# Kernel tuning notes

Hardware: AMD Instinct MI355X
Metric: run time of the kernel (lower is better)

The kernel has to match this reference:

```python
import jax, jax.numpy as jnp
import numpy as np

N, E = 50000, 800000
DIN, DH, DOUT = 128, 64, 16


def setup_inputs() -> dict:
    key = jax.random.key(0)
    ks = jax.random.split(key, 8)
    s = lambda d: np.float32(1.0 / np.sqrt(d))
    return {
        "x": jax.random.normal(ks[0], (N, DIN), jnp.float32),
        "edge_index": jax.random.randint(ks[1], (2, E), 0, N, dtype=jnp.int32),
        "w0": jax.random.normal(ks[2], (DIN, DH), jnp.float32) * s(DIN),
        "b0": jnp.zeros((DH,), jnp.float32),
        "w1": jax.random.normal(ks[3], (DH, DH), jnp.float32) * s(DH),
        "b1": jnp.zeros((DH,), jnp.float32),
        "w2": jax.random.normal(ks[4], (DH, DH), jnp.float32) * s(DH),
        "b2": jnp.zeros((DH,), jnp.float32),
        "fc_w": jax.random.normal(ks[5], (DH, DOUT), jnp.float32) * s(DH),
        "fc_b": jnp.zeros((DOUT,), jnp.float32),
    }


def reference(x, edge_index, w0, b0, w1, b1, w2, b2, fc_w, fc_b):
    n = x.shape[0]
    loop = jnp.arange(n, dtype=edge_index.dtype)
    # PyG GCNConv default: add self-loops, symmetric normalization
    src = jnp.concatenate([edge_index[0], loop])  # [E+N]
    dst = jnp.concatenate([edge_index[1], loop])
    deg = jax.ops.segment_sum(jnp.ones_like(dst, dtype=x.dtype), dst, num_segments=n)
    dinv = jnp.where(deg > 0, jax.lax.rsqrt(deg), 0.0)
    norm = dinv[src] * dinv[dst]  # [E+N]

    def conv(h, W, b):
        h = h @ W                            # [N, DH]
        msg = h[src] * norm[:, None]         # [E+N, DH] gather + scale
        return jax.ops.segment_sum(msg, dst, num_segments=n) + b

    h = jax.nn.elu(conv(x, w0, b0))
    h = jax.nn.elu(conv(h, w1, b1))
    h = jax.nn.elu(conv(h, w2, b2))
    return jax.nn.softmax(h @ fc_w + fc_b, axis=1)
```

## Files before the change

kernel.cpp:

```cpp
#include <hip/hip_runtime.h>
#include <hip/hip_fp16.h>
#include <math.h>

#define DIN 128
#define DH  64
#define DOUT 16
#define NWIN 8

typedef _Float16 f16x8 __attribute__((ext_vector_type(8)));
typedef float f32x4 __attribute__((ext_vector_type(4)));

__global__ __launch_bounds__(256) void deg_kernel(const int* __restrict__ dst,
                                                  int* __restrict__ counts, int E) {
    int e = blockIdx.x * 256 + threadIdx.x;
    if (e < E) atomicAdd(&counts[dst[e]], 1);
}

__global__ __launch_bounds__(256) void alloc_kernel(const int* __restrict__ counts,
                                                    int* __restrict__ gtotal,
                                                    int* __restrict__ offs,
                                                    int* __restrict__ cursor,
                                                    float* __restrict__ dinv, int n) {
    int i = blockIdx.x * 256 + threadIdx.x;
    if (i >= n) return;
    int c = counts[i];
    int pad = (c + 7) & ~7;
    int o = atomicAdd(gtotal, pad);
    offs[i] = o;
    cursor[i] = o;
    dinv[i] = rsqrtf((float)(c + 1));
}

__global__ __launch_bounds__(256) void fill_kernel(int* __restrict__ a, int v, int cap) {
    int i = blockIdx.x * 256 + threadIdx.x;
    if (i < cap) a[i] = v;
}

__global__ __launch_bounds__(256) void scatter_kernel(const int* __restrict__ src,
                                                      const int* __restrict__ dst,
                                                      int* __restrict__ cursor,
                                                      int* __restrict__ csr_src,
                                                      int E, int winSize) {
    int win = blockIdx.x & (NWIN - 1);
    int group = blockIdx.x >> 3;
    int nGroups = gridDim.x >> 3;
    int lo = win * winSize, hi = lo + winSize;
    int stride = nGroups * 256;
    for (int e = group * 256 + threadIdx.x; e < E; e += stride) {
        int d = dst[e];
        if (d >= lo && d < hi) {
            int j = atomicAdd(&cursor[d], 1);
            csr_src[j] = src[e];
        }
    }
}

__global__ __launch_bounds__(256) void mm128_mfma(const float* __restrict__ H,
                                                  const float* __restrict__ W,
                                                  const float* __restrict__ dinv,
                                                  __half* __restrict__ T, int n, int nTiles) {
    __shared__ _Float16 bhi[4][4][64][8];
    __shared__ _Float16 blo[4][4][64][8];
    int tid = threadIdx.x;
    for (int it = 0; it < 32; ++it) {
        int idx = it * 256 + tid;
        int k = idx >> 6, nn = idx & 63;
        float w = W[idx];
        _Float16 h = (_Float16)w;
        _Float16 l = (_Float16)(w - (float)h);
        int kt = k >> 5, kr = k & 31;
        int g = kr >> 3, j = kr & 7;
        int ct = nn >> 4, c = nn & 15;
        int ln = g * 16 + c;
        bhi[kt][ct][ln][j] = h;
        blo[kt][ct][ln][j] = l;
    }
    if (blockIdx.x == 0 && tid < 64) T[(size_t)n * 64 + tid] = __float2half(0.f);
    __syncthreads();

    int wave = blockIdx.x * 4 + (tid >> 6);
    if (wave >= nTiles) return;
    int lane = tid & 63;
    f16x8 Bh[4][4], Bl[4][4];
    #pragma unroll
    for (int kt = 0; kt < 4; ++kt)
        #pragma unroll
        for (int ct = 0; ct < 4; ++ct) {
            Bh[kt][ct] = *(const f16x8*)&bhi[kt][ct][lane][0];
            Bl[kt][ct] = *(const f16x8*)&blo[kt][ct][lane][0];
        }
    int row0 = wave * 16;
    int arow = row0 + (lane & 15);
    if (arow >= n) arow = n - 1;
    const float* hp = H + (size_t)arow * 128 + ((lane >> 4) << 3);
    f32x4 acc[4];
    #pragma unroll
    for (int ct = 0; ct < 4; ++ct) acc[ct] = (f32x4){0.f, 0.f, 0.f, 0.f};
    #pragma unroll
    for (int kt = 0; kt < 4; ++kt) {
        float4 p0 = *(const float4*)(hp + kt * 32);
        float4 p1 = *(const float4*)(hp + kt * 32 + 4);
        float v[8] = {p0.x, p0.y, p0.z, p0.w, p1.x, p1.y, p1.z, p1.w};
        f16x8 ah, al;
        #pragma unroll
        for (int j = 0; j < 8; ++j) {
            _Float16 h = (_Float16)v[j];
            ah[j] = h;
            al[j] = (_Float16)(v[j] - (float)h);
        }
        #pragma unroll
        for (int ct = 0; ct < 4; ++ct) {
            acc[ct] = __builtin_amdgcn_mfma_f32_16x16x32_f16(ah, Bh[kt][ct], acc[ct], 0, 0, 0);
            acc[ct] = __builtin_amdgcn_mfma_f32_16x16x32_f16(al, Bh[kt][ct], acc[ct], 0, 0, 0);
            acc[ct] = __builtin_amdgcn_mfma_f32_16x16x32_f16(ah, Bl[kt][ct], acc[ct], 0, 0, 0);
        }
    }
    int rbase = row0 + ((lane >> 4) << 2);
    int cbase = lane & 15;
    #pragma unroll
    for (int r = 0; r < 4; ++r) {
        int row = rbase + r;
        if (row < n) {
            float d = dinv[row];
            #pragma unroll
            for (int ct = 0; ct < 4; ++ct)
                T[(size_t)row * 64 + ct * 16 + cbase] = __float2half(acc[ct][r] * d);
        }
    }
}

__global__ __launch_bounds__(256) void aggmm_kernel(const __half* __restrict__ T,
                                                    const int* __restrict__ offs,
                                                    const int* __restrict__ cnt,
                                                    const int* __restrict__ csr_src,
                                                    const float* __restrict__ dinv,
                                                    const float* __restrict__ bias,
                                                    const float* __restrict__ Wn,
                                                    __half* __restrict__ out, int n) {
    __shared__ __align__(16) float wl[64 * 64];
    __shared__ __align__(16) float rowbuf[8][68];
    int tid = threadIdx.x;
    for (int i = tid; i < 64 * 64; i += 256) wl[i] = Wn[i];
    if (blockIdx.x == 0 && tid < 64) out[(size_t)n * 64 + tid] = __float2half(0.f);
    __syncthreads();
    int hw = tid >> 5;
    int f2 = tid & 31;
    int node = blockIdx.x * 8 + hw;
    if (node >= n) return;

    const __half2* T2 = reinterpret_cast<const __half2*>(T);
    float di = dinv[node];
    int e0 = offs[node];
    int e1 = e0 + ((cnt[node] + 7) & ~7);
    float2 sv = __half22float2(T2[(size_t)node * 32 + f2]);
    float ax0 = sv.x, ay0 = sv.y;
    float ax1=0, ay1=0, ax2=0, ay2=0, ax3=0, ay3=0;
    #pragma unroll 1
    for (int e = e0; e < e1; e += 8) {
        int4 sa = *reinterpret_cast<const int4*>(&csr_src[e]);
        int4 sb = *reinterpret_cast<const int4*>(&csr_src[e + 4]);
        float2 v0 = __half22float2(T2[(size_t)sa.x * 32 + f2]);
        float2 v1 = __half22float2(T2[(size_t)sa.y * 32 + f2]);
        float2 v2 = __half22float2(T2[(size_t)sa.z * 32 + f2]);
        float2 v3 = __half22float2(T2[(size_t)sa.w * 32 + f2]);
        float2 v4 = __half22float2(T2[(size_t)sb.x * 32 + f2]);
        float2 v5 = __half22float2(T2[(size_t)sb.y * 32 + f2]);
        float2 v6 = __half22float2(T2[(size_t)sb.z * 32 + f2]);
        float2 v7 = __half22float2(T2[(size_t)sb.w * 32 + f2]);
        ax0 += v0.x + v4.x;  ay0 += v0.y + v4.y;
        ax1 += v1.x + v5.x;  ay1 += v1.y + v5.y;
        ax2 += v2.x + v6.x;  ay2 += v2.y + v6.y;
        ax3 += v3.x + v7.x;  ay3 += v3.y + v7.y;
    }
    float hx = (ax0 + ax1) + (ax2 + ax3);
    float hy = (ay0 + ay1) + (ay2 + ay3);
    float2 bv = *reinterpret_cast<const float2*>(&bias[2 * f2]);
    hx = hx * di + bv.x;
    hy = hy * di + bv.y;
    hx = hx > 0.f ? hx : expm1f(hx);
    hy = hy > 0.f ? hy : expm1f(hy);

    *reinterpret_cast<float2*>(&rowbuf[hw][2 * f2]) = make_float2(hx, hy);
    float ox = 0.f, oy = 0.f;
    #pragma unroll
    for (int k0 = 0; k0 < 64; k0 += 4) {
        float4 r4 = *reinterpret_cast<const float4*>(&rowbuf[hw][k0]);
        float2 w0 = *reinterpret_cast<const float2*>(&wl[(k0 + 0) * 64 + 2 * f2]);
        float2 w1 = *reinterpret_cast<const float2*>(&wl[(k0 + 1) * 64 + 2 * f2]);
        float2 w2 = *reinterpret_cast<const float2*>(&wl[(k0 + 2) * 64 + 2 * f2]);
        float2 w3 = *reinterpret_cast<const float2*>(&wl[(k0 + 3) * 64 + 2 * f2]);
        ox = fmaf(r4.x, w0.x, ox); oy = fmaf(r4.x, w0.y, oy);
        ox = fmaf(r4.y, w1.x, ox); oy = fmaf(r4.y, w1.y, oy);
        ox = fmaf(r4.z, w2.x, ox); oy = fmaf(r4.z, w2.y, oy);
        ox = fmaf(r4.w, w3.x, ox); oy = fmaf(r4.w, w3.y, oy);
    }
    __half2* out2 = reinterpret_cast<__half2*>(out);
    out2[(size_t)node * 32 + f2] = __float22half2_rn(make_float2(ox * di, oy * di));
}

__global__ __launch_bounds__(256) void aggfc_kernel(const __half* __restrict__ T,
                                                    const int* __restrict__ offs,
                                                    const int* __restrict__ cnt,
                                                    const int* __restrict__ csr_src,
                                                    const float* __restrict__ dinv,
                                                    const float* __restrict__ bias,
                                                    const float* __restrict__ fcw,
                                                    const float* __restrict__ fcb,
                                                    float* __restrict__ out, int n) {
    __shared__ __align__(16) float wl[64 * 17];
    __shared__ __align__(16) float rowbuf[8][68];
    int tid = threadIdx.x;
    for (int i = tid; i < 64 * 16; i += 256) {
        int k = i >> 4, j = i & 15;
        wl[k * 17 + j] = fcw[i];
    }
    __syncthreads();
    int hw = tid >> 5, f2 = tid & 31;
    int node = blockIdx.x * 8 + hw;
    if (node >= n) return;

    const __half2* T2 = reinterpret_cast<const __half2*>(T);
    float di = dinv[node];
    int e0 = offs[node];
    int e1 = e0 + ((cnt[node] + 7) & ~7);
    float2 sv = __half22float2(T2[(size_t)node * 32 + f2]);
    float ax0 = sv.x, ay0 = sv.y;
    float ax1=0, ay1=0, ax2=0, ay2=0, ax3=0, ay3=0;
    #pragma unroll 1
    for (int e = e0; e < e1; e += 8) {
        int4 sa = *reinterpret_cast<const int4*>(&csr_src[e]);
        int4 sb = *reinterpret_cast<const int4*>(&csr_src[e + 4]);
        float2 v0 = __half22float2(T2[(size_t)sa.x * 32 + f2]);
        float2 v1 = __half22float2(T2[(size_t)sa.y * 32 + f2]);
        float2 v2 = __half22float2(T2[(size_t)sa.z * 32 + f2]);
        float2 v3 = __half22float2(T2[(size_t)sa.w * 32 + f2]);
        float2 v4 = __half22float2(T2[(size_t)sb.x * 32 + f2]);
        float2 v5 = __half22float2(T2[(size_t)sb.y * 32 + f2]);
        float2 v6 = __half22float2(T2[(size_t)sb.z * 32 + f2]);
        float2 v7 = __half22float2(T2[(size_t)sb.w * 32 + f2]);
        ax0 += v0.x + v4.x;  ay0 += v0.y + v4.y;
        ax1 += v1.x + v5.x;  ay1 += v1.y + v5.y;
        ax2 += v2.x + v6.x;  ay2 += v2.y + v6.y;
        ax3 += v3.x + v7.x;  ay3 += v3.y + v7.y;
    }
    float hx = (ax0 + ax1) + (ax2 + ax3);
    float hy = (ay0 + ay1) + (ay2 + ay3);
    float2 bv = *reinterpret_cast<const float2*>(&bias[2 * f2]);
    hx = hx * di + bv.x;
    hy = hy * di + bv.y;
    hx = hx > 0.f ? hx : expm1f(hx);
    hy = hy > 0.f ? hy : expm1f(hy);
    *reinterpret_cast<float2*>(&rowbuf[hw][2 * f2]) = make_float2(hx, hy);

    int g = f2 >> 4;
    int j = f2 & 15;
    float o = 0.f;
    #pragma unroll
    for (int kk = 0; kk < 32; ++kk) {
        int k = g * 32 + kk;
        o += rowbuf[hw][k] * wl[k * 17 + j];
    }
    o += __shfl_xor(o, 16, 64);
    o += fcb[j];
    float m = o;
    #pragma unroll
    for (int d = 8; d; d >>= 1) m = fmaxf(m, __shfl_xor(m, d, 64));
    float ex = expf(o - m);
    float s = ex;
    #pragma unroll
    for (int d = 8; d; d >>= 1) s += __shfl_xor(s, d, 64);
    if ((f2 & 16) == 0) out[(size_t)node * 16 + j] = ex / s;
}

extern "C" void kernel_launch(void* const* d_in, const int* in_sizes, int n_in,
                              void* d_out, int out_size, void* d_ws, size_t ws_size,
                              hipStream_t stream) {
    const float* x   = (const float*)d_in[0];
    const int*   ei  = (const int*)d_in[1];
    const float* w0  = (const float*)d_in[2];
    const float* b0  = (const float*)d_in[3];
    const float* w1  = (const float*)d_in[4];
    const float* b1  = (const float*)d_in[5];
    const float* w2  = (const float*)d_in[6];
    const float* b2  = (const float*)d_in[7];
    const float* fcw = (const float*)d_in[8];
    const float* fcb = (const float*)d_in[9];
    float* out = (float*)d_out;

    const int N = in_sizes[0] / DIN;
    const int E = in_sizes[1] / 2;
    const int* src = ei;
    const int* dst = ei + E;
    const int csr_cap = E + 8 * N + 8;

    char* p = (char*)d_ws;
    auto take = [&](size_t bytes) {
        char* q = p;
        p += (bytes + 255) & ~(size_t)255;
        return q;
    };
    int*    counts  = (int*)take((size_t)(N + 1) * 4);
    int*    gtotal  = counts + N;
    int*    offs    = (int*)take((size_t)N * 4);
    int*    cursor  = (int*)take((size_t)N * 4);
    float*  dinv    = (float*)take((size_t)N * 4);
    int*    csr_src = (int*)take((size_t)csr_cap * 4);
    __half* tbufA   = (__half*)take((size_t)(N + 1) * DH * 2);
    __half* tbufB   = (__half*)take((size_t)(N + 1) * DH * 2);

    hipMemsetAsync(counts, 0, (size_t)(N + 1) * 4, stream);

    deg_kernel<<<(E + 255) / 256, 256, 0, stream>>>(dst, counts, E);
    alloc_kernel<<<(N + 255) / 256, 256, 0, stream>>>(counts, gtotal, offs, cursor, dinv, N);
    fill_kernel<<<(csr_cap + 255) / 256, 256, 0, stream>>>(csr_src, N, csr_cap);
    int winSize = (N + NWIN - 1) / NWIN;
    scatter_kernel<<<1024, 256, 0, stream>>>(src, dst, cursor, csr_src, E, winSize);

    int node_grid = (N + 7) / 8;
    int nTiles = (N + 15) / 16;

    mm128_mfma<<<(nTiles + 3) / 4, 256, 0, stream>>>(x, w0, dinv, tbufA, N, nTiles);
    aggmm_kernel<<<node_grid, 256, 0, stream>>>(tbufA, offs, counts, csr_src,
                                                dinv, b0, w1, tbufB, N);
    aggmm_kernel<<<node_grid, 256, 0, stream>>>(tbufB, offs, counts, csr_src,
                                                dinv, b1, w2, tbufA, N);
    aggfc_kernel<<<node_grid, 256, 0, stream>>>(tbufA, offs, counts, csr_src,
                                                dinv, b2, fcw, fcb, out, N);
}
```

Before: 278.2 us.

## Split feature tables into column halves and gather each half separately

Splits each transformed feature table into two 32-column fp16 halves stored in separate buffers, so every gather pass touches a 3.2 MB table that can stay resident in cache instead of a 6.4 MB one. Aggregation is split in two: one kernel gathers the first half into an fp32 scratch buffer, and a second kernel gathers the other half, combines both, applies ELU and runs the next layer's matmul on MFMA (split fp16 hi/lo) over 64-node tiles. The final layer's FC and softmax also move to MFMA. This doubles the passes over the CSR index array, adds extra kernel launches and an fp32 scratch round-trip, and uses nontemporal hints on the index loads.

```diff
diff --git a/kernel.cpp b/kernel.cpp
--- a/kernel.cpp
+++ b/kernel.cpp
@@ -2,13 +2,12 @@
 #include <hip/hip_fp16.h>
 #include <math.h>
 
-#define DIN 128
-#define DH  64
-#define DOUT 16
 #define NWIN 8
 
 typedef _Float16 f16x8 __attribute__((ext_vector_type(8)));
 typedef float f32x4 __attribute__((ext_vector_type(4)));
+
+__device__ __forceinline__ float eluf(float v) { return v > 0.f ? v : expm1f(v); }
 
 __global__ __launch_bounds__(256) void deg_kernel(const int* __restrict__ dst,
                                                   int* __restrict__ counts, int E) {
@@ -58,7 +57,9 @@
 __global__ __launch_bounds__(256) void mm128_mfma(const float* __restrict__ H,
                                                   const float* __restrict__ W,
                                                   const float* __restrict__ dinv,
-                                                  __half* __restrict__ T, int n, int nTiles) {
+                                                  __half* __restrict__ TA,
+                                                  __half* __restrict__ TB,
+                                                  int n, int nTiles) {
     __shared__ _Float16 bhi[4][4][64][8];
     __shared__ _Float16 blo[4][4][64][8];
     int tid = threadIdx.x;
@@ -71,11 +72,13 @@
         int kt = k >> 5, kr = k & 31;
         int g = kr >> 3, j = kr & 7;
         int ct = nn >> 4, c = nn & 15;
-        int ln = g * 16 + c;
-        bhi[kt][ct][ln][j] = h;
-        blo[kt][ct][ln][j] = l;
-    }
-    if (blockIdx.x == 0 && tid < 64) T[(size_t)n * 64 + tid] = __float2half(0.f);
+        bhi[kt][ct][g * 16 + c][j] = h;
+        blo[kt][ct][g * 16 + c][j] = l;
+    }
+    if (blockIdx.x == 0 && tid < 32) {
+        TA[n * 32 + tid] = __float2half(0.f);
+        TB[n * 32 + tid] = __float2half(0.f);
+    }
     __syncthreads();
 
     int wave = blockIdx.x * 4 + (tid >> 6);
@@ -123,153 +126,311 @@
         if (row < n) {
             float d = dinv[row];
             #pragma unroll
-            for (int ct = 0; ct < 4; ++ct)
-                T[(size_t)row * 64 + ct * 16 + cbase] = __float2half(acc[ct][r] * d);
-        }
-    }
-}
-
-__global__ __launch_bounds__(256) void aggmm_kernel(const __half* __restrict__ T,
-                                                    const int* __restrict__ offs,
-                                                    const int* __restrict__ cnt,
-                                                    const int* __restrict__ csr_src,
-                                                    const float* __restrict__ dinv,
-                                                    const float* __restrict__ bias,
-                                                    const float* __restrict__ Wn,
-                                                    __half* __restrict__ out, int n) {
-    __shared__ __align__(16) float wl[64 * 64];
-    __shared__ __align__(16) float rowbuf[8][68];
-    int tid = threadIdx.x;
-    for (int i = tid; i < 64 * 64; i += 256) wl[i] = Wn[i];
-    if (blockIdx.x == 0 && tid < 64) out[(size_t)n * 64 + tid] = __float2half(0.f);
-    __syncthreads();
-    int hw = tid >> 5;
-    int f2 = tid & 31;
-    int node = blockIdx.x * 8 + hw;
+            for (int ct = 0; ct < 4; ++ct) {
+                int col = ct * 16 + cbase;
+                __half* P = (col < 32) ? TA : TB;
+                P[row * 32 + (col & 31)] = __float2half(acc[ct][r] * d);
+            }
+        }
+    }
+}
+
+__global__ __launch_bounds__(256) void gatherA_kernel(const __half* __restrict__ P,
+                                                      const int* __restrict__ offs,
+                                                      const int* __restrict__ cnt,
+                                                      const int* __restrict__ csr_src,
+                                                      float* __restrict__ agg, int n) {
+    int t = blockIdx.x * 256 + threadIdx.x;
+    int node = t >> 4, l = t & 15;
     if (node >= n) return;
-
-    const __half2* T2 = reinterpret_cast<const __half2*>(T);
-    float di = dinv[node];
+    const __half2* P2 = (const __half2*)P;
+    float2 sv = __half22float2(P2[node * 16 + l]);
+    float ax0 = sv.x, ay0 = sv.y;
+    float ax1 = 0, ay1 = 0, ax2 = 0, ay2 = 0, ax3 = 0, ay3 = 0;
     int e0 = offs[node];
     int e1 = e0 + ((cnt[node] + 7) & ~7);
-    float2 sv = __half22float2(T2[(size_t)node * 32 + f2]);
-    float ax0 = sv.x, ay0 = sv.y;
-    float ax1=0, ay1=0, ax2=0, ay2=0, ax3=0, ay3=0;
     #pragma unroll 1
     for (int e = e0; e < e1; e += 8) {
-        int4 sa = *reinterpret_cast<const int4*>(&csr_src[e]);
-        int4 sb = *reinterpret_cast<const int4*>(&csr_src[e + 4]);
-        float2 v0 = __half22float2(T2[(size_t)sa.x * 32 + f2]);
-        float2 v1 = __half22float2(T2[(size_t)sa.y * 32 + f2]);
-        float2 v2 = __half22float2(T2[(size_t)sa.z * 32 + f2]);
-        float2 v3 = __half22float2(T2[(size_t)sa.w * 32 + f2]);
-        float2 v4 = __half22float2(T2[(size_t)sb.x * 32 + f2]);
-        float2 v5 = __half22float2(T2[(size_t)sb.y * 32 + f2]);
-        float2 v6 = __half22float2(T2[(size_t)sb.z * 32 + f2]);
-        float2 v7 = __half22float2(T2[(size_t)sb.w * 32 + f2]);
+        int s0 = __builtin_nontemporal_load(csr_src + e);
+        int s1 = __builtin_nontemporal_load(csr_src + e + 1);
+        int s2 = __builtin_nontemporal_load(csr_src + e + 2);
+        int s3 = __builtin_nontemporal_load(csr_src + e + 3);
+        int s4 = __builtin_nontemporal_load(csr_src + e + 4);
+        int s5 = __builtin_nontemporal_load(csr_src + e + 5);
+        int s6 = __builtin_nontemporal_load(csr_src + e + 6);
+        int s7 = __builtin_nontemporal_load(csr_src + e + 7);
+        float2 v0 = __half22float2(P2[s0 * 16 + l]);
+        float2 v1 = __half22float2(P2[s1 * 16 + l]);
+        float2 v2 = __half22float2(P2[s2 * 16 + l]);
+        float2 v3 = __half22float2(P2[s3 * 16 + l]);
+        float2 v4 = __half22float2(P2[s4 * 16 + l]);
+        float2 v5 = __half22float2(P2[s5 * 16 + l]);
+        float2 v6 = __half22float2(P2[s6 * 16 + l]);
+        float2 v7 = __half22float2(P2[s7 * 16 + l]);
         ax0 += v0.x + v4.x;  ay0 += v0.y + v4.y;
         ax1 += v1.x + v5.x;  ay1 += v1.y + v5.y;
         ax2 += v2.x + v6.x;  ay2 += v2.y + v6.y;
         ax3 += v3.x + v7.x;  ay3 += v3.y + v7.y;
     }
-    float hx = (ax0 + ax1) + (ax2 + ax3);
-    float hy = (ay0 + ay1) + (ay2 + ay3);
-    float2 bv = *reinterpret_cast<const float2*>(&bias[2 * f2]);
-    hx = hx * di + bv.x;
-    hy = hy * di + bv.y;
-    hx = hx > 0.f ? hx : expm1f(hx);
-    hy = hy > 0.f ? hy : expm1f(hy);
-
-    *reinterpret_cast<float2*>(&rowbuf[hw][2 * f2]) = make_float2(hx, hy);
-    float ox = 0.f, oy = 0.f;
-    #pragma unroll
-    for (int k0 = 0; k0 < 64; k0 += 4) {
-        float4 r4 = *reinterpret_cast<const float4*>(&rowbuf[hw][k0]);
-        float2 w0 = *reinterpret_cast<const float2*>(&wl[(k0 + 0) * 64 + 2 * f2]);
-        float2 w1 = *reinterpret_cast<const float2*>(&wl[(k0 + 1) * 64 + 2 * f2]);
-        float2 w2 = *reinterpret_cast<const float2*>(&wl[(k0 + 2) * 64 + 2 * f2]);
-        float2 w3 = *reinterpret_cast<const float2*>(&wl[(k0 + 3) * 64 + 2 * f2]);
-        ox = fmaf(r4.x, w0.x, ox); oy = fmaf(r4.x, w0.y, oy);
-        ox = fmaf(r4.y, w1.x, ox); oy = fmaf(r4.y, w1.y, oy);
-        ox = fmaf(r4.z, w2.x, ox); oy = fmaf(r4.z, w2.y, oy);
-        ox = fmaf(r4.w, w3.x, ox); oy = fmaf(r4.w, w3.y, oy);
-    }
-    __half2* out2 = reinterpret_cast<__half2*>(out);
-    out2[(size_t)node * 32 + f2] = __float22half2_rn(make_float2(ox * di, oy * di));
-}
-
-__global__ __launch_bounds__(256) void aggfc_kernel(const __half* __restrict__ T,
-                                                    const int* __restrict__ offs,
-                                                    const int* __restrict__ cnt,
-                                                    const int* __restrict__ csr_src,
-                                                    const float* __restrict__ dinv,
-                                                    const float* __restrict__ bias,
-                                                    const float* __restrict__ fcw,
-                                                    const float* __restrict__ fcb,
-                                                    float* __restrict__ out, int n) {
-    __shared__ __align__(16) float wl[64 * 17];
-    __shared__ __align__(16) float rowbuf[8][68];
+    float rx = (ax0 + ax1) + (ax2 + ax3);
+    float ry = (ay0 + ay1) + (ay2 + ay3);
+    __builtin_nontemporal_store(rx, agg + node * 32 + 2 * l);
+    __builtin_nontemporal_store(ry, agg + node * 32 + 2 * l + 1);
+}
+
+__global__ __launch_bounds__(256, 4) void gatherB_mm(const __half* __restrict__ PB,
+                                                     const float* __restrict__ agg,
+                                                     const int* __restrict__ offs,
+                                                     const int* __restrict__ cnt,
+                                                     const int* __restrict__ csr_src,
+                                                     const float* __restrict__ dinv,
+                                                     const float* __restrict__ bias,
+                                                     const float* __restrict__ Wn,
+                                                     __half* __restrict__ outA,
+                                                     __half* __restrict__ outB, int n) {
+    __shared__ _Float16 bhi[2][4][64][8];
+    __shared__ _Float16 blo[2][4][64][8];
+    __shared__ float rowbuf[64][68];
     int tid = threadIdx.x;
-    for (int i = tid; i < 64 * 16; i += 256) {
-        int k = i >> 4, j = i & 15;
-        wl[k * 17 + j] = fcw[i];
+    for (int it = 0; it < 16; ++it) {
+        int idx = it * 256 + tid;
+        int k = idx >> 6, nn = idx & 63;
+        float w = Wn[idx];
+        _Float16 h = (_Float16)w;
+        _Float16 lo = (_Float16)(w - (float)h);
+        int kt = k >> 5, kr = k & 31;
+        int g = kr >> 3, j = kr & 7;
+        int ct = nn >> 4, c = nn & 15;
+        bhi[kt][ct][g * 16 + c][j] = h;
+        blo[kt][ct][g * 16 + c][j] = lo;
+    }
+    if (blockIdx.x == 0 && tid < 32) {
+        outA[n * 32 + tid] = __float2half(0.f);
+        outB[n * 32 + tid] = __float2half(0.f);
+    }
+    int g16 = tid >> 4, l = tid & 15;
+    int nodebase = blockIdx.x * 64;
+    const __half2* P2 = (const __half2*)PB;
+    #pragma unroll 1
+    for (int q = 0; q < 4; ++q) {
+        int ln = 4 * g16 + q;
+        int node = nodebase + ln;
+        float h0 = 0.f, h1 = 0.f, h2 = 0.f, h3 = 0.f;
+        if (node < n) {
+            float2 sv = __half22float2(P2[node * 16 + l]);
+            float ax0 = sv.x, ay0 = sv.y;
+            float ax1 = 0, ay1 = 0, ax2 = 0, ay2 = 0, ax3 = 0, ay3 = 0;
+            int e0 = offs[node];
+            int e1 = e0 + ((cnt[node] + 7) & ~7);
+            #pragma unroll 1
+            for (int e = e0; e < e1; e += 8) {
+                int s0 = __builtin_nontemporal_load(csr_src + e);
+                int s1 = __builtin_nontemporal_load(csr_src + e + 1);
+                int s2 = __builtin_nontemporal_load(csr_src + e + 2);
+                int s3 = __builtin_nontemporal_load(csr_src + e + 3);
+                int s4 = __builtin_nontemporal_load(csr_src + e + 4);
+                int s5 = __builtin_nontemporal_load(csr_src + e + 5);
+                int s6 = __builtin_nontemporal_load(csr_src + e + 6);
+                int s7 = __builtin_nontemporal_load(csr_src + e + 7);
+                float2 v0 = __half22float2(P2[s0 * 16 + l]);
+                float2 v1 = __half22float2(P2[s1 * 16 + l]);
+                float2 v2 = __half22float2(P2[s2 * 16 + l]);
+                float2 v3 = __half22float2(P2[s3 * 16 + l]);
+                float2 v4 = __half22float2(P2[s4 * 16 + l]);
+                float2 v5 = __half22float2(P2[s5 * 16 + l]);
+                float2 v6 = __half22float2(P2[s6 * 16 + l]);
+                float2 v7 = __half22float2(P2[s7 * 16 + l]);
+                ax0 += v0.x + v4.x;  ay0 += v0.y + v4.y;
+                ax1 += v1.x + v5.x;  ay1 += v1.y + v5.y;
+                ax2 += v2.x + v6.x;  ay2 += v2.y + v6.y;
+                ax3 += v3.x + v7.x;  ay3 += v3.y + v7.y;
+            }
+            float shx = (ax0 + ax1) + (ax2 + ax3);
+            float shy = (ay0 + ay1) + (ay2 + ay3);
+            float a0 = __builtin_nontemporal_load(agg + node * 32 + 2 * l);
+            float a1 = __builtin_nontemporal_load(agg + node * 32 + 2 * l + 1);
+            float di = dinv[node];
+            float2 bl = *(const float2*)(bias + 2 * l);
+            float2 bh = *(const float2*)(bias + 32 + 2 * l);
+            h0 = eluf(a0 * di + bl.x);
+            h1 = eluf(a1 * di + bl.y);
+            h2 = eluf(shx * di + bh.x);
+            h3 = eluf(shy * di + bh.y);
+        }
+        *(float2*)&rowbuf[ln][2 * l] = make_float2(h0, h1);
+        *(float2*)&rowbuf[ln][32 + 2 * l] = make_float2(h2, h3);
     }
     __syncthreads();
-    int hw = tid >> 5, f2 = tid & 31;
-    int node = blockIdx.x * 8 + hw;
-    if (node >= n) return;
-
-    const __half2* T2 = reinterpret_cast<const __half2*>(T);
-    float di = dinv[node];
-    int e0 = offs[node];
-    int e1 = e0 + ((cnt[node] + 7) & ~7);
-    float2 sv = __half22float2(T2[(size_t)node * 32 + f2]);
-    float ax0 = sv.x, ay0 = sv.y;
-    float ax1=0, ay1=0, ax2=0, ay2=0, ax3=0, ay3=0;
+
+    int wv = tid >> 6, lane = tid & 63;
+    f16x8 Bh[2][4], Bl[2][4];
+    #pragma unroll
+    for (int kt = 0; kt < 2; ++kt)
+        #pragma unroll
+        for (int ct = 0; ct < 4; ++ct) {
+            Bh[kt][ct] = *(const f16x8*)&bhi[kt][ct][lane][0];
+            Bl[kt][ct] = *(const f16x8*)&blo[kt][ct][lane][0];
+        }
+    int trow = wv * 16 + (lane & 15);
+    int kb = (lane >> 4) << 3;
+    f32x4 acc[4];
+    #pragma unroll
+    for (int ct = 0; ct < 4; ++ct) acc[ct] = (f32x4){0.f, 0.f, 0.f, 0.f};
+    #pragma unroll
+    for (int kt = 0; kt < 2; ++kt) {
+        float4 p0 = *(const float4*)&rowbuf[trow][kt * 32 + kb];
+        float4 p1 = *(const float4*)&rowbuf[trow][kt * 32 + kb + 4];
+        float v[8] = {p0.x, p0.y, p0.z, p0.w, p1.x, p1.y, p1.z, p1.w};
+        f16x8 ah, al;
+        #pragma unroll
+        for (int j = 0; j < 8; ++j) {
+            _Float16 h = (_Float16)v[j];
+            ah[j] = h;
+            al[j] = (_Float16)(v[j] - (float)h);
+        }
+        #pragma unroll
+        for (int ct = 0; ct < 4; ++ct) {
+            acc[ct] = __builtin_amdgcn_mfma_f32_16x16x32_f16(ah, Bh[kt][ct], acc[ct], 0, 0, 0);
+            acc[ct] = __builtin_amdgcn_mfma_f32_16x16x32_f16(al, Bh[kt][ct], acc[ct], 0, 0, 0);
+            acc[ct] = __builtin_amdgcn_mfma_f32_16x16x32_f16(ah, Bl[kt][ct], acc[ct], 0, 0, 0);
+        }
+    }
+    int rb = wv * 16 + ((lane >> 4) << 2);
+    int cb = lane & 15;
+    #pragma unroll
+    for (int r = 0; r < 4; ++r) {
+        int node = nodebase + rb + r;
+        if (node < n) {
+            float d = dinv[node];
+            #pragma unroll
+            for (int ct = 0; ct < 4; ++ct) {
+                int col = ct * 16 + cb;
+                __half* P = (col < 32) ? outA : outB;
+                P[node * 32 + (col & 31)] = __float2half(acc[ct][r] * d);
+            }
+        }
+    }
+}
+
+__global__ __launch_bounds__(256, 4) void gatherB_fc(const __half* __restrict__ PB,
+                                                     const float* __restrict__ agg,
+                                                     const int* __restrict__ offs,
+                                                     const int* __restrict__ cnt,
+                                                     const int* __restrict__ csr_src,
+                                                     const float* __restrict__ dinv,
+                                                     const float* __restrict__ bias,
+                                                     const float* __restrict__ fcw,
+                                                     const float* __restrict__ fcb,
+                                                     float* __restrict__ out, int n) {
+    __shared__ _Float16 bhi[2][64][8];
+    __shared__ _Float16 blo[2][64][8];
+    __shared__ float rowbuf[64][68];
+    int tid = threadIdx.x;
+    for (int it = 0; it < 4; ++it) {
+        int idx = it * 256 + tid;
+        int k = idx >> 4, j16 = idx & 15;
+        float w = fcw[idx];
+        _Float16 h = (_Float16)w;
+        _Float16 lo = (_Float16)(w - (float)h);
+        int kt = k >> 5, kr = k & 31;
+        int g = kr >> 3, j = kr & 7;
+        bhi[kt][g * 16 + j16][j] = h;
+        blo[kt][g * 16 + j16][j] = lo;
+    }
+    int g16 = tid >> 4, l = tid & 15;
+    int nodebase = blockIdx.x * 64;
+    const __half2* P2 = (const __half2*)PB;
     #pragma unroll 1
-    for (int e = e0; e < e1; e += 8) {
-        int4 sa = *reinterpret_cast<const int4*>(&csr_src[e]);
-        int4 sb = *reinterpret_cast<const int4*>(&csr_src[e + 4]);
-        float2 v0 = __half22float2(T2[(size_t)sa.x * 32 + f2]);
-        float2 v1 = __half22float2(T2[(size_t)sa.y * 32 + f2]);
-        float2 v2 = __half22float2(T2[(size_t)sa.z * 32 + f2]);
-        float2 v3 = __half22float2(T2[(size_t)sa.w * 32 + f2]);
-        float2 v4 = __half22float2(T2[(size_t)sb.x * 32 + f2]);
-        float2 v5 = __half22float2(T2[(size_t)sb.y * 32 + f2]);
-        float2 v6 = __half22float2(T2[(size_t)sb.z * 32 + f2]);
-        float2 v7 = __half22float2(T2[(size_t)sb.w * 32 + f2]);
-        ax0 += v0.x + v4.x;  ay0 += v0.y + v4.y;
-        ax1 += v1.x + v5.x;  ay1 += v1.y + v5.y;
-        ax2 += v2.x + v6.x;  ay2 += v2.y + v6.y;
-        ax3 += v3.x + v7.x;  ay3 += v3.y + v7.y;
-    }
-    float hx = (ax0 + ax1) + (ax2 + ax3);
-    float hy = (ay0 + ay1) + (ay2 + ay3);
-    float2 bv = *reinterpret_cast<const float2*>(&bias[2 * f2]);
-    hx = hx * di + bv.x;
-    hy = hy * di + bv.y;
-    hx = hx > 0.f ? hx : expm1f(hx);
-    hy = hy > 0.f ? hy : expm1f(hy);
-    *reinterpret_cast<float2*>(&rowbuf[hw][2 * f2]) = make_float2(hx, hy);
-
-    int g = f2 >> 4;
-    int j = f2 & 15;
-    float o = 0.f;
-    #pragma unroll
-    for (int kk = 0; kk < 32; ++kk) {
-        int k = g * 32 + kk;
-        o += rowbuf[hw][k] * wl[k * 17 + j];
-    }
-    o += __shfl_xor(o, 16, 64);
-    o += fcb[j];
-    float m = o;
-    #pragma unroll
-    for (int d = 8; d; d >>= 1) m = fmaxf(m, __shfl_xor(m, d, 64));
-    float ex = expf(o - m);
-    float s = ex;
-    #pragma unroll
-    for (int d = 8; d; d >>= 1) s += __shfl_xor(s, d, 64);
-    if ((f2 & 16) == 0) out[(size_t)node * 16 + j] = ex / s;
+    for (int q = 0; q < 4; ++q) {
+        int ln = 4 * g16 + q;
+        int node = nodebase + ln;
+        float h0 = 0.f, h1 = 0.f, h2 = 0.f, h3 = 0.f;
+        if (node < n) {
+            float2 sv = __half22float2(P2[node * 16 + l]);
+            float ax0 = sv.x, ay0 = sv.y;
+            float ax1 = 0, ay1 = 0, ax2 = 0, ay2 = 0, ax3 = 0, ay3 = 0;
+            int e0 = offs[node];
+            int e1 = e0 + ((cnt[node] + 7) & ~7);
+            #pragma unroll 1
+            for (int e = e0; e < e1; e += 8) {
+                int s0 = __builtin_nontemporal_load(csr_src + e);
+                int s1 = __builtin_nontemporal_load(csr_src + e + 1);
+                int s2 = __builtin_nontemporal_load(csr_src + e + 2);
+                int s3 = __builtin_nontemporal_load(csr_src + e + 3);
+                int s4 = __builtin_nontemporal_load(csr_src + e + 4);
+                int s5 = __builtin_nontemporal_load(csr_src + e + 5);
+                int s6 = __builtin_nontemporal_load(csr_src + e + 6);
+                int s7 = __builtin_nontemporal_load(csr_src + e + 7);
+                float2 v0 = __half22float2(P2[s0 * 16 + l]);
+                float2 v1 = __half22float2(P2[s1 * 16 + l]);
+                float2 v2 = __half22float2(P2[s2 * 16 + l]);
+                float2 v3 = __half22float2(P2[s3 * 16 + l]);
+                float2 v4 = __half22float2(P2[s4 * 16 + l]);
+                float2 v5 = __half22float2(P2[s5 * 16 + l]);
+                float2 v6 = __half22float2(P2[s6 * 16 + l]);
+                float2 v7 = __half22float2(P2[s7 * 16 + l]);
+                ax0 += v0.x + v4.x;  ay0 += v0.y + v4.y;
+                ax1 += v1.x + v5.x;  ay1 += v1.y + v5.y;
+                ax2 += v2.x + v6.x;  ay2 += v2.y + v6.y;
+                ax3 += v3.x + v7.x;  ay3 += v3.y + v7.y;
+            }
+            float shx = (ax0 + ax1) + (ax2 + ax3);
+            float shy = (ay0 + ay1) + (ay2 + ay3);
+            float a0 = __builtin_nontemporal_load(agg + node * 32 + 2 * l);
+            float a1 = __builtin_nontemporal_load(agg + node * 32 + 2 * l + 1);
+            float di = dinv[node];
+            float2 bl = *(const float2*)(bias + 2 * l);
+            float2 bh = *(const float2*)(bias + 32 + 2 * l);
+            h0 = eluf(a0 * di + bl.x);
+            h1 = eluf(a1 * di + bl.y);
+            h2 = eluf(shx * di + bh.x);
+            h3 = eluf(shy * di + bh.y);
+        }
+        *(float2*)&rowbuf[ln][2 * l] = make_float2(h0, h1);
+        *(float2*)&rowbuf[ln][32 + 2 * l] = make_float2(h2, h3);
+    }
+    __syncthreads();
+
+    int wv = tid >> 6, lane = tid & 63;
+    f16x8 Bh[2], Bl[2];
+    #pragma unroll
+    for (int kt = 0; kt < 2; ++kt) {
+        Bh[kt] = *(const f16x8*)&bhi[kt][lane][0];
+        Bl[kt] = *(const f16x8*)&blo[kt][lane][0];
+    }
+    int trow = wv * 16 + (lane & 15);
+    int kb = (lane >> 4) << 3;
+    f32x4 acc = (f32x4){0.f, 0.f, 0.f, 0.f};
+    #pragma unroll
+    for (int kt = 0; kt < 2; ++kt) {
+        float4 p0 = *(const float4*)&rowbuf[trow][kt * 32 + kb];
+        float4 p1 = *(const float4*)&rowbuf[trow][kt * 32 + kb + 4];
+        float v[8] = {p0.x, p0.y, p0.z, p0.w, p1.x, p1.y, p1.z, p1.w};
+        f16x8 ah, al;
+        #pragma unroll
+        for (int j = 0; j < 8; ++j) {
+            _Float16 h = (_Float16)v[j];
+            ah[j] = h;
+            al[j] = (_Float16)(v[j] - (float)h);
+        }
+        acc = __builtin_amdgcn_mfma_f32_16x16x32_f16(ah, Bh[kt], acc, 0, 0, 0);
+        acc = __builtin_amdgcn_mfma_f32_16x16x32_f16(al, Bh[kt], acc, 0, 0, 0);
+        acc = __builtin_amdgcn_mfma_f32_16x16x32_f16(ah, Bl[kt], acc, 0, 0, 0);
+    }
+    float bj = fcb[lane & 15];
+    #pragma unroll
+    for (int r = 0; r < 4; ++r) {
+        float o = acc[r] + bj;
+        float m = o;
+        #pragma unroll
+        for (int d = 8; d; d >>= 1) m = fmaxf(m, __shfl_xor(m, d, 64));
+        float ex = expf(o - m);
+        float s = ex;
+        #pragma unroll
+        for (int d = 8; d; d >>= 1) s += __shfl_xor(s, d, 64);
+        int node = nodebase + wv * 16 + ((lane >> 4) << 2) + r;
+        if (node < n) out[(size_t)node * 16 + (lane & 15)] = ex / s;
+    }
 }
 
 extern "C" void kernel_launch(void* const* d_in, const int* in_sizes, int n_in,
@@ -287,7 +448,7 @@
     const float* fcb = (const float*)d_in[9];
     float* out = (float*)d_out;
 
-    const int N = in_sizes[0] / DIN;
+    const int N = in_sizes[0] / 128;
     const int E = in_sizes[1] / 2;
     const int* src = ei;
     const int* dst = ei + E;
@@ -305,8 +466,11 @@
     int*    cursor  = (int*)take((size_t)N * 4);
     float*  dinv    = (float*)take((size_t)N * 4);
     int*    csr_src = (int*)take((size_t)csr_cap * 4);
-    __half* tbufA   = (__half*)take((size_t)(N + 1) * DH * 2);
-    __half* tbufB   = (__half*)take((size_t)(N + 1) * DH * 2);
+    float*  aggbuf  = (float*)take((size_t)N * 32 * 4);
+    __half* TA0     = (__half*)take((size_t)(N + 1) * 32 * 2);
+    __half* TB0     = (__half*)take((size_t)(N + 1) * 32 * 2);
+    __half* TA1     = (__half*)take((size_t)(N + 1) * 32 * 2);
+    __half* TB1     = (__half*)take((size_t)(N + 1) * 32 * 2);
 
     hipMemsetAsync(counts, 0, (size_t)(N + 1) * 4, stream);
 
@@ -316,14 +480,19 @@
     int winSize = (N + NWIN - 1) / NWIN;
     scatter_kernel<<<1024, 256, 0, stream>>>(src, dst, cursor, csr_src, E, winSize);
 
-    int node_grid = (N + 7) / 8;
     int nTiles = (N + 15) / 16;
-
-    mm128_mfma<<<(nTiles + 3) / 4, 256, 0, stream>>>(x, w0, dinv, tbufA, N, nTiles);
-    aggmm_kernel<<<node_grid, 256, 0, stream>>>(tbufA, offs, counts, csr_src,
-                                                dinv, b0, w1, tbufB, N);
-    aggmm_kernel<<<node_grid, 256, 0, stream>>>(tbufB, offs, counts, csr_src,
-                                                dinv, b1, w2, tbufA, N);
-    aggfc_kernel<<<node_grid, 256, 0, stream>>>(tbufA, offs, counts, csr_src,
-                                                dinv, b2, fcw, fcb, out, N);
-}
+    int gA_grid = (N + 15) / 16;
+    int gB_grid = (N + 63) / 64;
+
+    mm128_mfma<<<(nTiles + 3) / 4, 256, 0, stream>>>(x, w0, dinv, TA0, TB0, N, nTiles);
+
+    gatherA_kernel<<<gA_grid, 256, 0, stream>>>(TA0, offs, counts, csr_src, aggbuf, N);
+    gatherB_mm<<<gB_grid, 256, 0, stream>>>(TB0, aggbuf, offs, counts, csr_src,
+                                            dinv, b0, w1, TA1, TB1, N);
+    gatherA_kernel<<<gA_grid, 256, 0, stream>>>(TA1, offs, counts, csr_src, aggbuf, N);
+    gatherB_mm<<<gB_grid, 256, 0, stream>>>(TB1, aggbuf, offs, counts, csr_src,
+                                            dinv, b1, w2, TA0, TB0, N);
+    gatherA_kernel<<<gA_grid, 256, 0, stream>>>(TA0, offs, counts, csr_src, aggbuf, N);
+    gatherB_fc<<<gB_grid, 256, 0, stream>>>(TB0, aggbuf, offs, counts, csr_src,
+                                            dinv, b2, fcw, fcb, out, N);
+}
```

After: 306.7 us. +10.3%, slower.
